# Performance work log

Hardware: AMD Instinct MI355X
Metric: run time of the kernel (lower is better)

## Reference

```python
import jax, jax.numpy as jnp
import numpy as np

VOCAB, D, E, B, S = 32000, 1024, 4, 4, 1024
DF = 4 * D  # Expert.internal_dim = d_model * 4


def setup_inputs() -> dict:
    key = jax.random.key(0)
    ks = jax.random.split(key, 14)
    sc = 0.02
    return {
        "tokens": jax.random.randint(ks[0], (B, S), 0, VOCAB),
        "emb": jax.random.normal(ks[1], (VOCAB, D), jnp.float32) * sc,
        "Wih": jax.random.normal(ks[2], (D, D), jnp.float32) * sc,
        "bih": jnp.zeros((D,), jnp.float32),
        "Whh": jax.random.normal(ks[3], (D, D), jnp.float32) * sc,
        "bhh": jnp.zeros((D,), jnp.float32),
        "Wg": jax.random.normal(ks[4], (E, D), jnp.float32) * sc,
        "W1": jax.random.normal(ks[5], (E, D, DF), jnp.float32) * sc,
        "b1": jnp.zeros((E, DF), jnp.float32),
        "W2": jax.random.normal(ks[6], (E, DF, D), jnp.float32) * sc,
        "b2": jnp.zeros((E, D), jnp.float32),
        "Wfc": jax.random.normal(ks[7], (VOCAB, D), jnp.float32) * sc,
        "bfc": jnp.zeros((VOCAB,), jnp.float32),
    }


def reference(tokens, emb, Wih, bih, Whh, bhh, Wg, W1, b1, W2, b2, Wfc, bfc):
    # token embedding: [B,S,D]
    x = emb[tokens]

    # nn.RNN(batch_first=True), tanh nonlinearity, h0 = zeros (h=None path)
    def step(h, xt):
        h = jnp.tanh(xt @ Wih.T + bih + h @ Whh.T + bhh)
        return h, h

    h0 = jnp.zeros((x.shape[0], x.shape[-1]), x.dtype)
    h_last, hs = jax.lax.scan(step, h0, jnp.swapaxes(x, 0, 1))  # hs: [S,B,D]
    x = jnp.swapaxes(hs, 0, 1)  # [B,S,D]

    # DarwinianRouter on pooled sequence repr: softmax gate, top_k=1
    gates = jax.nn.softmax(x.mean(axis=1) @ Wg.T, axis=-1)  # [B,E]
    w, idx = jax.lax.top_k(gates, 1)  # [B,1] each
    idx0 = idx[:, 0]

    # OuroborosMoE dispatch: per-sequence top-1 expert MLP, scaled by gate weight.
    # Gather per-batch expert params instead of boolean-mask gather/scatter loop.
    W1g, b1g = W1[idx0], b1[idx0]          # [B,D,DF], [B,DF]
    W2g, b2g = W2[idx0], b2[idx0]          # [B,DF,D], [B,D]
    h1 = jax.nn.gelu(jnp.einsum('bsd,bdf->bsf', x, W1g) + b1g[:, None, :], approximate=False)
    y = (jnp.einsum('bsf,bfd->bsd', h1, W2g) + b2g[:, None, :]) * w[:, :, None]  # [B,S,D]

    logits = y @ Wfc.T + bfc  # [B,S,VOCAB]
    return logits


if __name__ == "__main__":
    out = reference(**setup_inputs())
    print(out.shape)
```

## Files before the change

kernel.cpp:

```cpp
#include <hip/hip_runtime.h>
#include <hip/hip_bf16.h>
#include <math.h>

#define DD    1024
#define SS    1024
#define BB    4
#define EE    4
#define DFF   4096
#define VOC   32000

typedef __attribute__((ext_vector_type(8))) short v8s;
typedef __attribute__((ext_vector_type(4))) float v4f;

__device__ __forceinline__ unsigned short f2b(float f) {
    unsigned u = __float_as_uint(f);
    unsigned r = (u + 0x7FFFu + ((u >> 16) & 1u)) >> 16;
    return (unsigned short)r;
}
__device__ __forceinline__ float b2f(unsigned short h) {
    return __uint_as_float((unsigned)h << 16);
}

__device__ __forceinline__ void xcd_swizzle(int& bx, int& by) {
    int gx = gridDim.x;
    int nwg = gx * gridDim.y;
    int id = by * gx + bx;
    int q = nwg >> 3, r = nwg & 7;
    int xcd = id & 7, o = id >> 3;
    int swz = (xcd < r ? xcd * (q + 1) : r * (q + 1) + (xcd - r) * q) + o;
    bx = swz % gx; by = swz / gx;
}

template<bool GATHER>
__global__ __launch_bounds__(256)
void split_cast(const float* __restrict__ src, const int* __restrict__ tokens,
                unsigned short* __restrict__ Xhi, unsigned short* __restrict__ Xlo)
{
    const int row = blockIdx.x;
    const float4* s;
    if constexpr (GATHER)
        s = (const float4*)(src + (size_t)tokens[row] * DD);
    else
        s = (const float4*)(src + (size_t)row * DD);
    const int c = threadIdx.x;
    float4 v = s[c];
    ushort4 hi, lo;
    hi.x = f2b(v.x); hi.y = f2b(v.y); hi.z = f2b(v.z); hi.w = f2b(v.w);
    lo.x = f2b(v.x - b2f(hi.x)); lo.y = f2b(v.y - b2f(hi.y));
    lo.z = f2b(v.z - b2f(hi.z)); lo.w = f2b(v.w - b2f(hi.w));
    ((ushort4*)Xhi)[(size_t)row * 256 + c] = hi;
    ((ushort4*)Xlo)[(size_t)row * 256 + c] = lo;
}

__global__ __launch_bounds__(1024)
void rnn_kernel(const float* __restrict__ U,
                const float* __restrict__ Whh,
                float*       __restrict__ HS,
                unsigned long long* __restrict__ hpair,
                float*       __restrict__ MEANX)
{
    __shared__ float hs_s[2][4 * 1088];

    const int tid = threadIdx.x;
    const int g = blockIdx.x;
    const int out = tid >> 4;
    const int chunk = tid & 15;
    const int b = out >> 4;
    const int dl = out & 15;
    const int d_own = g * 16 + dl;
    const bool is_res = (chunk == 0);

    float4 wreg[16];
    #pragma unroll
    for (int j = 0; j < 16; ++j)
        wreg[j] = *(const float4*)(Whh + (size_t)d_own * DD + chunk * 64 + j * 4);

    const int sb = tid >> 8;
    const int sk = (tid & 255) * 4;
    const int sks = sk + ((sk >> 6) << 2);
    const int rofs = b * 1088 + chunk * 68;

    float m_acc = 0.f;

    for (int t = 0; t < SS; ++t) {
        float u_pre = 0.f;
        if (is_res)
            u_pre = U[((size_t)(b * SS + t)) * DD + d_own];

        const int par = t & 1;
        if (t > 0) {
            const char* pb = (const char*)(hpair + (size_t)((t - 1) & 1) * 4096)
                             + tid * 32;
            uint4 q0, q1;
            const unsigned tg = (unsigned)t;
            for (;;) {
                asm volatile(
                    "global_load_dwordx4 %0, %2, off sc0 sc1\n\t"
                    "global_load_dwordx4 %1, %2, off offset:16 sc0 sc1\n\t"
                    "s_waitcnt vmcnt(0)"
                    : "=&v"(q0), "=&v"(q1)
                    : "v"(pb)
                    : "memory");
                if ((q0.y == tg) & (q0.w == tg) & (q1.y == tg) & (q1.w == tg))
                    break;
                __builtin_amdgcn_s_sleep(1);
            }
            *(float4*)&hs_s[par][sb * 1088 + sks] = make_float4(
                __uint_as_float(q0.x), __uint_as_float(q0.z),
                __uint_as_float(q1.x), __uint_as_float(q1.z));
        }
        __syncthreads();

        float acc = 0.f;
        if (t > 0) {
            const float* rbase = &hs_s[par][rofs];
            #pragma unroll
            for (int j = 0; j < 16; ++j) {
                float4 h4 = *(const float4*)(rbase + j * 4);
                float4 w4 = wreg[j];
                acc += w4.x * h4.x + w4.y * h4.y + w4.z * h4.z + w4.w * h4.w;
            }
            acc += __shfl_xor(acc, 1);
            acc += __shfl_xor(acc, 2);
            acc += __shfl_xor(acc, 4);
            acc += __shfl_xor(acc, 8);
        }

        if (is_res) {
            float h = tanhf(u_pre + acc);
            HS[((size_t)(b * SS + t)) * DD + d_own] = h;
            m_acc += h;
            unsigned long long pk =
                ((unsigned long long)(unsigned)(t + 1) << 32) |
                (unsigned long long)__float_as_uint(h);
            __hip_atomic_store(&hpair[(size_t)(t & 1) * 4096 + b * 1024 + d_own],
                               pk, __ATOMIC_RELAXED, __HIP_MEMORY_SCOPE_AGENT);
        }
    }

    if (is_res)
        MEANX[b * DD + d_own] = m_acc * (1.0f / (float)SS);
}

__global__ __launch_bounds__(256)
void gate_kernel(const float* __restrict__ MEANX, const float* __restrict__ Wg,
                 float* __restrict__ WGATE, int* __restrict__ IDX)
{
    __shared__ float sc[4][4];
    const int tid = threadIdx.x;
    const int p = tid >> 4, l = tid & 15;
    const int b = p >> 2, e = p & 3;
    float acc = 0.f;
    for (int j = 0; j < 64; ++j)
        acc += MEANX[b * DD + l * 64 + j] * Wg[e * DD + l * 64 + j];
    acc += __shfl_xor(acc, 1); acc += __shfl_xor(acc, 2);
    acc += __shfl_xor(acc, 4); acc += __shfl_xor(acc, 8);
    if (l == 0) sc[b][e] = acc;
    __syncthreads();
    if (tid < 4) {
        float s0 = sc[tid][0], s1 = sc[tid][1], s2 = sc[tid][2], s3 = sc[tid][3];
        float mx = fmaxf(fmaxf(s0, s1), fmaxf(s2, s3));
        float e0 = expf(s0 - mx), e1 = expf(s1 - mx);
        float e2 = expf(s2 - mx), e3 = expf(s3 - mx);
        float inv = 1.0f / (e0 + e1 + e2 + e3);
        float pr[4] = {e0 * inv, e1 * inv, e2 * inv, e3 * inv};
        int arg = 0; float best = pr[0];
        if (pr[1] > best) { best = pr[1]; arg = 1; }
        if (pr[2] > best) { best = pr[2]; arg = 2; }
        if (pr[3] > best) { best = pr[3]; arg = 3; }
        WGATE[tid] = best;
        IDX[tid] = arg;
    }
}

__global__ __launch_bounds__(256)
void cast_kernel(const float* __restrict__ in, unsigned short* __restrict__ out,
                 long long n4)
{
    long long stride = (long long)gridDim.x * blockDim.x;
    for (long long i = (long long)blockIdx.x * blockDim.x + threadIdx.x;
         i < n4; i += stride) {
        float4 v = ((const float4*)in)[i];
        ushort4 o;
        o.x = f2b(v.x); o.y = f2b(v.y); o.z = f2b(v.z); o.w = f2b(v.w);
        ((ushort4*)out)[i] = o;
    }
}

__global__ __launch_bounds__(256)
void transpose_cast(const float* __restrict__ src, const int* __restrict__ expIdx,
                    unsigned short* __restrict__ dst, int R, int C,
                    long long srcExpStride, long long dstZStride)
{
    __shared__ float tbuf[32][33];
    const int tid = threadIdx.x;
    const int z = blockIdx.z;
    const float* S = src + (long long)expIdx[z] * srcExpStride;
    unsigned short* D = dst + (long long)z * dstZStride;
    const int r0 = blockIdx.y * 32, c0 = blockIdx.x * 32;
    const int tr = tid >> 3, tc = (tid & 7) * 4;
    float4 v = *(const float4*)(S + (long long)(r0 + tr) * C + c0 + tc);
    tbuf[tr][tc + 0] = v.x; tbuf[tr][tc + 1] = v.y;
    tbuf[tr][tc + 2] = v.z; tbuf[tr][tc + 3] = v.w;
    __syncthreads();
    ushort4 o;
    o.x = f2b(tbuf[tc + 0][tr]); o.y = f2b(tbuf[tc + 1][tr]);
    o.z = f2b(tbuf[tc + 2][tr]); o.w = f2b(tbuf[tc + 3][tr]);
    *(ushort4*)(D + (long long)(c0 + tr) * R + r0 + tc) = o;
}

__device__ __forceinline__ void load_lds16(const void* g, void* l) {
    __builtin_amdgcn_global_load_lds(
        (const __attribute__((address_space(1))) unsigned int*)g,
        (__attribute__((address_space(3))) unsigned int*)l, 16, 0, 0);
}

template<int EPI>
__global__ __launch_bounds__(256)
void gemm_bf16(const unsigned short* __restrict__ A,
               const unsigned short* __restrict__ Bt,
               const float* __restrict__ bias,
               void* __restrict__ Cv,
               int N, int K,
               long long aStride, long long cStride, long long btStride,
               const float* __restrict__ scaleP, const int* __restrict__ expIdx)
{
    __shared__ __align__(16) unsigned short Asm[128 * 32];
    __shared__ __align__(16) unsigned short Bsm[128 * 32];

    const int tid = threadIdx.x;
    const int wave = tid >> 6, lane = tid & 63;
    int bxs = blockIdx.x, bys = blockIdx.y;
    xcd_swizzle(bxs, bys);
    const int bm = bys * 128, bn = bxs * 128;
    const int bz = blockIdx.z;
    const int wm = (wave >> 1) * 64, wn = (wave & 1) * 64;
    const int fr = lane & 15, kh = lane >> 4;

    const unsigned short* Az  = A  + (long long)bz * aStride;
    const unsigned short* Btz = Bt + (long long)bz * btStride;
    const float* bp = bias + (expIdx ? (long long)expIdx[bz] * N : 0);

    const int lo0 = wave * 1024 + lane * 16;
    const int lo1 = 4096 + lo0;
    const int r0 = lo0 >> 6, q0 = (lo0 & 63) >> 1;
    const int r1 = lo1 >> 6, q1 = (lo1 & 63) >> 1;
    const unsigned short* a0 = Az  + (size_t)(bm + r0) * K + q0;
    const unsigned short* a1 = Az  + (size_t)(bm + r1) * K + q1;
    const unsigned short* b0 = Btz + (size_t)(bn + r0) * K + q0;
    const unsigned short* b1 = Btz + (size_t)(bn + r1) * K + q1;

    v4f acc[4][4];
    #pragma unroll
    for (int i = 0; i < 4; ++i)
        #pragma unroll
        for (int j = 0; j < 4; ++j) {
            acc[i][j][0] = 0.f; acc[i][j][1] = 0.f;
            acc[i][j][2] = 0.f; acc[i][j][3] = 0.f;
        }

    for (int k0 = 0; k0 < K; k0 += 32) {
        load_lds16(a0 + k0, (char*)Asm + wave * 1024);
        load_lds16(a1 + k0, (char*)Asm + 4096 + wave * 1024);
        load_lds16(b0 + k0, (char*)Bsm + wave * 1024);
        load_lds16(b1 + k0, (char*)Bsm + 4096 + wave * 1024);
        __syncthreads();

        v8s af[4], bfv[4];
        #pragma unroll
        for (int f = 0; f < 4; ++f) {
            af[f]  = *(const v8s*)((const char*)Asm + ((wm + f * 16 + fr) << 6) + (kh << 4));
            bfv[f] = *(const v8s*)((const char*)Bsm + ((wn + f * 16 + fr) << 6) + (kh << 4));
        }
        #pragma unroll
        for (int fi = 0; fi < 4; ++fi)
            #pragma unroll
            for (int fj = 0; fj < 4; ++fj)
                acc[fi][fj] = __builtin_amdgcn_mfma_f32_16x16x32_bf16(
                    af[fi], bfv[fj], acc[fi][fj], 0, 0, 0);
        __syncthreads();
    }

    const float scale = (EPI == 2) ? scaleP[bz] : 1.0f;
    #pragma unroll
    for (int fi = 0; fi < 4; ++fi) {
        #pragma unroll
        for (int fj = 0; fj < 4; ++fj) {
            v4f t = acc[fi][fj];
            int col = bn + wn + fj * 16 + fr;
            float bb = bp[col];
            int rbase = bm + wm + fi * 16 + (kh << 2);
            #pragma unroll
            for (int r = 0; r < 4; ++r) {
                float v = t[r] + bb;
                if constexpr (EPI == 1)
                    v = 0.5f * v * (1.0f + erff(v * 0.70710678118654752440f));
                if constexpr (EPI == 2)
                    v *= scale;
                size_t off = (size_t)bz * (size_t)cStride +
                             (size_t)(rbase + r) * N + col;
                if constexpr (EPI == 0)
                    ((float*)Cv)[off] = v;
                else
                    ((unsigned short*)Cv)[off] = f2b(v);
            }
        }
    }
}

__global__ __launch_bounds__(256)
void gemm_bf16_split(const unsigned short* __restrict__ Ahi,
                     const unsigned short* __restrict__ Alo,
                     const unsigned short* __restrict__ Bhi,
                     const unsigned short* __restrict__ Blo,
                     const float* __restrict__ bias1,
                     const float* __restrict__ bias2,
                     float* __restrict__ C, int N, int K)
{
    __shared__ __align__(16) unsigned short AsmH[128 * 32];
    __shared__ __align__(16) unsigned short AsmL[128 * 32];
    __shared__ __align__(16) unsigned short BsmH[128 * 32];
    __shared__ __align__(16) unsigned short BsmL[128 * 32];

    const int tid = threadIdx.x;
    const int wave = tid >> 6, lane = tid & 63;
    int bxs = blockIdx.x, bys = blockIdx.y;
    xcd_swizzle(bxs, bys);
    const int bm = bys * 128, bn = bxs * 128;
    const int wm = (wave >> 1) * 64, wn = (wave & 1) * 64;
    const int fr = lane & 15, kh = lane >> 4;

    const int lo0 = wave * 1024 + lane * 16;
    const int lo1 = 4096 + lo0;
    const int r0 = lo0 >> 6, q0 = (lo0 & 63) >> 1;
    const int r1 = lo1 >> 6, q1 = (lo1 & 63) >> 1;
    const unsigned short* ah0 = Ahi + (size_t)(bm + r0) * K + q0;
    const unsigned short* ah1 = Ahi + (size_t)(bm + r1) * K + q1;
    const unsigned short* al0 = Alo + (size_t)(bm + r0) * K + q0;
    const unsigned short* al1 = Alo + (size_t)(bm + r1) * K + q1;
    const unsigned short* bh0 = Bhi + (size_t)(bn + r0) * K + q0;
    const unsigned short* bh1 = Bhi + (size_t)(bn + r1) * K + q1;
    const unsigned short* bl0 = Blo + (size_t)(bn + r0) * K + q0;
    const unsigned short* bl1 = Blo + (size_t)(bn + r1) * K + q1;

    v4f acc[4][4];
    #pragma unroll
    for (int i = 0; i < 4; ++i)
        #pragma unroll
        for (int j = 0; j < 4; ++j) {
            acc[i][j][0] = 0.f; acc[i][j][1] = 0.f;
            acc[i][j][2] = 0.f; acc[i][j][3] = 0.f;
        }

    for (int k0 = 0; k0 < K; k0 += 32) {
        load_lds16(ah0 + k0, (char*)AsmH + wave * 1024);
        load_lds16(ah1 + k0, (char*)AsmH + 4096 + wave * 1024);
        load_lds16(al0 + k0, (char*)AsmL + wave * 1024);
        load_lds16(al1 + k0, (char*)AsmL + 4096 + wave * 1024);
        load_lds16(bh0 + k0, (char*)BsmH + wave * 1024);
        load_lds16(bh1 + k0, (char*)BsmH + 4096 + wave * 1024);
        load_lds16(bl0 + k0, (char*)BsmL + wave * 1024);
        load_lds16(bl1 + k0, (char*)BsmL + 4096 + wave * 1024);
        __syncthreads();

        v8s ahf[4], alf[4];
        #pragma unroll
        for (int f = 0; f < 4; ++f) {
            int ao = ((wm + f * 16 + fr) << 6) + (kh << 4);
            ahf[f] = *(const v8s*)((const char*)AsmH + ao);
            alf[f] = *(const v8s*)((const char*)AsmL + ao);
        }
        #pragma unroll
        for (int fj = 0; fj < 4; ++fj) {
            int bo = ((wn + fj * 16 + fr) << 6) + (kh << 4);
            v8s bh = *(const v8s*)((const char*)BsmH + bo);
            v8s bl = *(const v8s*)((const char*)BsmL + bo);
            #pragma unroll
            for (int fi = 0; fi < 4; ++fi) {
                acc[fi][fj] = __builtin_amdgcn_mfma_f32_16x16x32_bf16(
                    alf[fi], bh, acc[fi][fj], 0, 0, 0);
                acc[fi][fj] = __builtin_amdgcn_mfma_f32_16x16x32_bf16(
                    ahf[fi], bl, acc[fi][fj], 0, 0, 0);
                acc[fi][fj] = __builtin_amdgcn_mfma_f32_16x16x32_bf16(
                    ahf[fi], bh, acc[fi][fj], 0, 0, 0);
            }
        }
        __syncthreads();
    }

    #pragma unroll
    for (int fi = 0; fi < 4; ++fi) {
        #pragma unroll
        for (int fj = 0; fj < 4; ++fj) {
            v4f t = acc[fi][fj];
            int col = bn + wn + fj * 16 + fr;
            float bb = bias1[col] + bias2[col];
            int rbase = bm + wm + fi * 16 + (kh << 2);
            #pragma unroll
            for (int r = 0; r < 4; ++r)
                C[(size_t)(rbase + r) * N + col] = t[r] + bb;
        }
    }
}

extern "C" void kernel_launch(void* const* d_in, const int* in_sizes, int n_in,
                              void* d_out, int out_size, void* d_ws, size_t ws_size,
                              hipStream_t stream)
{
    const int*   tokens = (const int*)  d_in[0];
    const float* emb    = (const float*)d_in[1];
    const float* Wih    = (const float*)d_in[2];
    const float* bih    = (const float*)d_in[3];
    const float* Whh    = (const float*)d_in[4];
    const float* bhh    = (const float*)d_in[5];
    const float* Wg     = (const float*)d_in[6];
    const float* W1     = (const float*)d_in[7];
    const float* b1     = (const float*)d_in[8];
    const float* W2     = (const float*)d_in[9];
    const float* b2     = (const float*)d_in[10];
    const float* Wfc    = (const float*)d_in[11];
    const float* bfc    = (const float*)d_in[12];
    float* out = (float*)d_out;
    float* ws  = (float*)d_ws;

    float*          U     = ws;
    float*          HS    = ws + 4194304;
    unsigned short* HSbf  = (unsigned short*)(ws + 8388608);
    float*          Ebase = ws + 10485760;
    float*          Fbase = ws + 18874368;
    unsigned short* Ybf   = (unsigned short*)(ws + 27262976);
    float*          MEANX = ws + 29360128;
    float*          WGATE = ws + 29364224;
    int*            IDX   = (int*)(ws + 29364228);
    unsigned short* Xhi   = (unsigned short*)Ebase;
    unsigned short* Xlo   = (unsigned short*)(Ebase + 2097152);
    unsigned short* Whi   = (unsigned short*)(Ebase + 4194304);
    unsigned short* Wlo   = (unsigned short*)(Ebase + 4718592);
    unsigned long long* HPAIR = (unsigned long long*)Fbase;
    unsigned short* W1T   = (unsigned short*)Ebase;
    unsigned short* W2T   = (unsigned short*)Ebase;
    unsigned short* H1bf  = (unsigned short*)Fbase;
    unsigned short* Wfcbf = (unsigned short*)Ebase;

    hipMemsetAsync(HPAIR, 0, 2 * 4096 * sizeof(unsigned long long), stream);

    split_cast<true ><<<BB * SS, 256, 0, stream>>>(emb, tokens, Xhi, Xlo);
    split_cast<false><<<DD, 256, 0, stream>>>(Wih, nullptr, Whi, Wlo);

    gemm_bf16_split<<<dim3(DD / 128, (BB * SS) / 128, 1), 256, 0, stream>>>(
        Xhi, Xlo, Whi, Wlo, bih, bhh, U, DD, DD);

    rnn_kernel<<<64, 1024, 0, stream>>>(U, Whh, HS, HPAIR, MEANX);

    gate_kernel<<<1, 256, 0, stream>>>(MEANX, Wg, WGATE, IDX);

    cast_kernel<<<1024, 256, 0, stream>>>(HS, HSbf, (long long)(BB * SS) * DD / 4);

    transpose_cast<<<dim3(DFF / 32, DD / 32, BB), 256, 0, stream>>>(
        W1, IDX, W1T, DD, DFF, (long long)DD * DFF, (long long)DFF * DD);

    gemm_bf16<1><<<dim3(DFF / 128, SS / 128, BB), 256, 0, stream>>>(
        HSbf, W1T, b1, H1bf, DFF, DD,
        (long long)SS * DD, (long long)SS * DFF, (long long)DFF * DD,
        nullptr, IDX);

    transpose_cast<<<dim3(DD / 32, DFF / 32, BB), 256, 0, stream>>>(
        W2, IDX, W2T, DFF, DD, (long long)DFF * DD, (long long)DD * DFF);

    gemm_bf16<2><<<dim3(DD / 128, SS / 128, BB), 256, 0, stream>>>(
        H1bf, W2T, b2, Ybf, DD, DFF,
        (long long)SS * DFF, (long long)SS * DD, (long long)DD * DFF,
        WGATE, IDX);

    cast_kernel<<<4096, 256, 0, stream>>>(Wfc, Wfcbf, (long long)VOC * DD / 4);

    gemm_bf16<0><<<dim3(VOC / 128, (BB * SS) / 128, 1), 256, 0, stream>>>(
        Ybf, Wfcbf, bfc, out, VOC, DD, 0, 0, 0, nullptr, nullptr);
}
```

Before: 2.824 ms.

## Split RNN blocks per batch row and write bf16 hidden states directly

Each RNN block now owns one batch row and 64 output dims instead of all four batch rows with 16 dims. Each block therefore polls only its own batch row's hidden state, one 8-byte load per thread instead of 32 bytes. The kernel writes the bf16 hidden-state sequence directly, which removes the separate fp32 store and the later cast kernel. The handshake buffer moves into the freed HS region. The trade is that each block still reads a different 64-row slice of Whh per batch, which quadruples total weight reads, though that happens only at load time.

```diff
diff --git a/kernel.cpp b/kernel.cpp
--- a/kernel.cpp
+++ b/kernel.cpp
@@ -55,71 +55,74 @@
 __global__ __launch_bounds__(1024)
 void rnn_kernel(const float* __restrict__ U,
                 const float* __restrict__ Whh,
-                float*       __restrict__ HS,
+                unsigned short* __restrict__ HSbf,
                 unsigned long long* __restrict__ hpair,
-                float*       __restrict__ MEANX)
-{
-    __shared__ float hs_s[2][4 * 1088];
+                float* __restrict__ MEANX)
+{
+    __shared__ float hs_s[2][1088];
 
     const int tid = threadIdx.x;
-    const int g = blockIdx.x;
+    const int b  = blockIdx.x >> 4;
+    const int gg = blockIdx.x & 15;
     const int out = tid >> 4;
     const int chunk = tid & 15;
-    const int b = out >> 4;
-    const int dl = out & 15;
-    const int d_own = g * 16 + dl;
+    const int d_own = gg * 64 + out;
     const bool is_res = (chunk == 0);
 
-    float4 wreg[16];
-    #pragma unroll
-    for (int j = 0; j < 16; ++j)
-        wreg[j] = *(const float4*)(Whh + (size_t)d_own * DD + chunk * 64 + j * 4);
-
-    const int sb = tid >> 8;
-    const int sk = (tid & 255) * 4;
-    const int sks = sk + ((sk >> 6) << 2);
-    const int rofs = b * 1088 + chunk * 68;
+    const float4* wrow = (const float4*)(Whh + (size_t)d_own * DD + chunk * 64);
+    float4 w00 = wrow[0],  w01 = wrow[1],  w02 = wrow[2],  w03 = wrow[3];
+    float4 w04 = wrow[4],  w05 = wrow[5],  w06 = wrow[6],  w07 = wrow[7];
+    float4 w08 = wrow[8],  w09 = wrow[9],  w10 = wrow[10], w11 = wrow[11];
+    float4 w12 = wrow[12], w13 = wrow[13], w14 = wrow[14], w15 = wrow[15];
+
+    const int sofs = tid + ((tid >> 6) << 2);
+    const int rofs = chunk * 68;
+    unsigned long long* hp_b = hpair + (size_t)b * 2048;
 
     float m_acc = 0.f;
 
     for (int t = 0; t < SS; ++t) {
+        const int par = t & 1;
         float u_pre = 0.f;
         if (is_res)
             u_pre = U[((size_t)(b * SS + t)) * DD + d_own];
 
-        const int par = t & 1;
         if (t > 0) {
-            const char* pb = (const char*)(hpair + (size_t)((t - 1) & 1) * 4096)
-                             + tid * 32;
-            uint4 q0, q1;
+            const unsigned long long* pp = hp_b + (size_t)((t - 1) & 1) * 1024 + tid;
+            uint2 q;
             const unsigned tg = (unsigned)t;
             for (;;) {
                 asm volatile(
-                    "global_load_dwordx4 %0, %2, off sc0 sc1\n\t"
-                    "global_load_dwordx4 %1, %2, off offset:16 sc0 sc1\n\t"
+                    "global_load_dwordx2 %0, %1, off sc0 sc1\n\t"
                     "s_waitcnt vmcnt(0)"
-                    : "=&v"(q0), "=&v"(q1)
-                    : "v"(pb)
-                    : "memory");
-                if ((q0.y == tg) & (q0.w == tg) & (q1.y == tg) & (q1.w == tg))
-                    break;
+                    : "=&v"(q) : "v"(pp) : "memory");
+                if (q.y == tg) break;
                 __builtin_amdgcn_s_sleep(1);
             }
-            *(float4*)&hs_s[par][sb * 1088 + sks] = make_float4(
-                __uint_as_float(q0.x), __uint_as_float(q0.z),
-                __uint_as_float(q1.x), __uint_as_float(q1.z));
+            hs_s[par][sofs] = __uint_as_float(q.x);
         }
         __syncthreads();
 
         float acc = 0.f;
         if (t > 0) {
-            const float* rbase = &hs_s[par][rofs];
-            #pragma unroll
-            for (int j = 0; j < 16; ++j) {
-                float4 h4 = *(const float4*)(rbase + j * 4);
-                float4 w4 = wreg[j];
-                acc += w4.x * h4.x + w4.y * h4.y + w4.z * h4.z + w4.w * h4.w;
-            }
+            const float* rb = &hs_s[par][rofs];
+            float4 h;
+            h = *(const float4*)(rb +  0); acc += w00.x*h.x + w00.y*h.y + w00.z*h.z + w00.w*h.w;
+            h = *(const float4*)(rb +  4); acc += w01.x*h.x + w01.y*h.y + w01.z*h.z + w01.w*h.w;
+            h = *(const float4*)(rb +  8); acc += w02.x*h.x + w02.y*h.y + w02.z*h.z + w02.w*h.w;
+            h = *(const float4*)(rb + 12); acc += w03.x*h.x + w03.y*h.y + w03.z*h.z + w03.w*h.w;
+            h = *(const float4*)(rb + 16); acc += w04.x*h.x + w04.y*h.y + w04.z*h.z + w04.w*h.w;
+            h = *(const float4*)(rb + 20); acc += w05.x*h.x + w05.y*h.y + w05.z*h.z + w05.w*h.w;
+            h = *(const float4*)(rb + 24); acc += w06.x*h.x + w06.y*h.y + w06.z*h.z + w06.w*h.w;
+            h = *(const float4*)(rb + 28); acc += w07.x*h.x + w07.y*h.y + w07.z*h.z + w07.w*h.w;
+            h = *(const float4*)(rb + 32); acc += w08.x*h.x + w08.y*h.y + w08.z*h.z + w08.w*h.w;
+            h = *(const float4*)(rb + 36); acc += w09.x*h.x + w09.y*h.y + w09.z*h.z + w09.w*h.w;
+            h = *(const float4*)(rb + 40); acc += w10.x*h.x + w10.y*h.y + w10.z*h.z + w10.w*h.w;
+            h = *(const float4*)(rb + 44); acc += w11.x*h.x + w11.y*h.y + w11.z*h.z + w11.w*h.w;
+            h = *(const float4*)(rb + 48); acc += w12.x*h.x + w12.y*h.y + w12.z*h.z + w12.w*h.w;
+            h = *(const float4*)(rb + 52); acc += w13.x*h.x + w13.y*h.y + w13.z*h.z + w13.w*h.w;
+            h = *(const float4*)(rb + 56); acc += w14.x*h.x + w14.y*h.y + w14.z*h.z + w14.w*h.w;
+            h = *(const float4*)(rb + 60); acc += w15.x*h.x + w15.y*h.y + w15.z*h.z + w15.w*h.w;
             acc += __shfl_xor(acc, 1);
             acc += __shfl_xor(acc, 2);
             acc += __shfl_xor(acc, 4);
@@ -128,13 +131,13 @@
 
         if (is_res) {
             float h = tanhf(u_pre + acc);
-            HS[((size_t)(b * SS + t)) * DD + d_own] = h;
+            HSbf[((size_t)(b * SS + t)) * DD + d_own] = f2b(h);
             m_acc += h;
             unsigned long long pk =
                 ((unsigned long long)(unsigned)(t + 1) << 32) |
                 (unsigned long long)__float_as_uint(h);
-            __hip_atomic_store(&hpair[(size_t)(t & 1) * 4096 + b * 1024 + d_own],
-                               pk, __ATOMIC_RELAXED, __HIP_MEMORY_SCOPE_AGENT);
+            __hip_atomic_store(hp_b + (size_t)par * 1024 + d_own, pk,
+                               __ATOMIC_RELAXED, __HIP_MEMORY_SCOPE_AGENT);
         }
     }
 
@@ -424,7 +427,7 @@
     float* ws  = (float*)d_ws;
 
     float*          U     = ws;
-    float*          HS    = ws + 4194304;
+    float*          HSdead= ws + 4194304;
     unsigned short* HSbf  = (unsigned short*)(ws + 8388608);
     float*          Ebase = ws + 10485760;
     float*          Fbase = ws + 18874368;
@@ -432,17 +435,18 @@
     float*          MEANX = ws + 29360128;
     float*          WGATE = ws + 29364224;
     int*            IDX   = (int*)(ws + 29364228);
+    unsigned long long* HPAIR = (unsigned long long*)HSdead;
     unsigned short* Xhi   = (unsigned short*)Ebase;
     unsigned short* Xlo   = (unsigned short*)(Ebase + 2097152);
     unsigned short* Whi   = (unsigned short*)(Ebase + 4194304);
     unsigned short* Wlo   = (unsigned short*)(Ebase + 4718592);
-    unsigned long long* HPAIR = (unsigned long long*)Fbase;
     unsigned short* W1T   = (unsigned short*)Ebase;
     unsigned short* W2T   = (unsigned short*)Ebase;
     unsigned short* H1bf  = (unsigned short*)Fbase;
     unsigned short* Wfcbf = (unsigned short*)Ebase;
 
-    hipMemsetAsync(HPAIR, 0, 2 * 4096 * sizeof(unsigned long long), stream);
+    hipMemsetAsync(HPAIR, 0, (size_t)BB * 2 * 1024 * sizeof(unsigned long long),
+                   stream);
 
     split_cast<true ><<<BB * SS, 256, 0, stream>>>(emb, tokens, Xhi, Xlo);
     split_cast<false><<<DD, 256, 0, stream>>>(Wih, nullptr, Whi, Wlo);
@@ -450,11 +454,9 @@
     gemm_bf16_split<<<dim3(DD / 128, (BB * SS) / 128, 1), 256, 0, stream>>>(
         Xhi, Xlo, Whi, Wlo, bih, bhh, U, DD, DD);
 
-    rnn_kernel<<<64, 1024, 0, stream>>>(U, Whh, HS, HPAIR, MEANX);
+    rnn_kernel<<<64, 1024, 0, stream>>>(U, Whh, HSbf, HPAIR, MEANX);
 
     gate_kernel<<<1, 256, 0, stream>>>(MEANX, Wg, WGATE, IDX);
-
-    cast_kernel<<<1024, 256, 0, stream>>>(HS, HSbf, (long long)(BB * SS) * DD / 4);
 
     transpose_cast<<<dim3(DFF / 32, DD / 32, BB), 256, 0, stream>>>(
         W1, IDX, W1T, DD, DFF, (long long)DD * DFF, (long long)DFF * DD);
```

Result: no change. 2.784 ms (-1.4%).
